# Kernel optimization log

Measured on AMD Instinct MI355X. Metric: run time of the kernel, lower is better.

Reference implementation:

```python
import jax, jax.numpy as jnp
import numpy as np

K_DIM = 256
HEADS = 8


def setup_inputs() -> dict:
    key = jax.random.key(0)
    ks = jax.random.split(key, 6)
    b, t, k, h = 8, 1024, K_DIM, HEADS
    scale = 1.0 / np.sqrt(k)
    x = jax.random.normal(ks[0], (b, t, k), dtype=jnp.float32)
    # nn.Linear(k, k*h, bias=False) weights, stored as (in, out) for x @ W
    Wq = jax.random.normal(ks[1], (k, k * h), dtype=jnp.float32) * scale
    Wk = jax.random.normal(ks[2], (k, k * h), dtype=jnp.float32) * scale
    Wv = jax.random.normal(ks[3], (k, k * h), dtype=jnp.float32) * scale
    # unifyheads: nn.Linear(h*k, k) with bias
    Wu = jax.random.normal(ks[4], (h * k, k), dtype=jnp.float32) * (1.0 / np.sqrt(h * k))
    bu = jax.random.normal(ks[5], (k,), dtype=jnp.float32) * 0.01
    return {"x": x, "Wq": Wq, "Wk": Wk, "Wv": Wv, "Wu": Wu, "bu": bu}


def reference(x, Wq, Wk, Wv, Wu, bu):
    b, t, k = x.shape
    h = Wq.shape[1] // k
    inv4 = 1.0 / (k ** 0.25)  # scale Q and K each by k^(1/4) -> combined 1/sqrt(k)
    q = (x @ Wq).reshape(b, t, h, k) * inv4
    kk = (x @ Wk).reshape(b, t, h, k) * inv4
    v = (x @ Wv).reshape(b, t, h, k)
    # scores: [b, h, t, t]
    scores = jnp.einsum('bthk,bshk->bhts', q, kk)
    att = jax.nn.softmax(scores, axis=-1)
    out = jnp.einsum('bhts,bshk->bthk', att, v).reshape(b, t, h * k)
    return out @ Wu + bu
```

## Files before the change

### kernel.cpp

```cpp
#include <hip/hip_runtime.h>
#include <stdint.h>

typedef unsigned short u16;
typedef __attribute__((ext_vector_type(8))) short bf16x8;
typedef __attribute__((ext_vector_type(4))) float f32x4;

#define LOG2E 1.44269504088896340736f

__device__ __forceinline__ float bf2f(u16 u) {
  union { uint32_t u; float f; } v; v.u = ((uint32_t)u) << 16; return v.f;
}
__device__ __forceinline__ u16 f2bf(float f) {
  union { float f; uint32_t u; } v; v.f = f;
  uint32_t r = v.u + 0x7fffu + ((v.u >> 16) & 1u);
  return (u16)(r >> 16);
}

__device__ __forceinline__ void gl_lds16(const u16* g, u16* l) {
  __builtin_amdgcn_global_load_lds((const __attribute__((address_space(1))) void*)g,
                                   (__attribute__((address_space(3))) void*)l, 16, 0, 0);
}

__device__ __forceinline__ void transpose64f(const float* src, int sstride,
                                             u16* dst, int dstride,
                                             float scale, u16* tile ) {
  const int tid = threadIdx.x;
  const int row = tid >> 3, seg = tid & 7;
#pragma unroll
  for (int p = 0; p < 2; ++p) {
    int rr = p * 32 + row;
    int rw = rr ^ (seg * 8);
    float4 a = *(const float4*)(src + rr * sstride + seg * 8);
    float4 b = *(const float4*)(src + rr * sstride + seg * 8 + 4);
    tile[(seg * 8 + 0) * 80 + rw] = f2bf(a.x * scale);
    tile[(seg * 8 + 1) * 80 + rw] = f2bf(a.y * scale);
    tile[(seg * 8 + 2) * 80 + rw] = f2bf(a.z * scale);
    tile[(seg * 8 + 3) * 80 + rw] = f2bf(a.w * scale);
    tile[(seg * 8 + 4) * 80 + rw] = f2bf(b.x * scale);
    tile[(seg * 8 + 5) * 80 + rw] = f2bf(b.y * scale);
    tile[(seg * 8 + 6) * 80 + rw] = f2bf(b.z * scale);
    tile[(seg * 8 + 7) * 80 + rw] = f2bf(b.w * scale);
  }
  __syncthreads();
#pragma unroll
  for (int p = 0; p < 2; ++p) {
    int rr = p * 32 + row;
    int sw = (seg ^ ((rr >> 3) & 7)) * 8;
    *(uint4*)(dst + rr * dstride + seg * 8) = *(uint4*)(tile + rr * 80 + sw);
  }
}

__global__ __launch_bounds__(256) void k_prep(const float* __restrict__ x,
                                              const float* __restrict__ Wq,
                                              const float* __restrict__ Wk,
                                              const float* __restrict__ Wv,
                                              const float* __restrict__ Wu,
                                              u16* __restrict__ xb,
                                              u16* __restrict__ Wt,
                                              u16* __restrict__ Wut) {
  __shared__ u16 tile[64 * 80];
  const int bx = blockIdx.x;
  if (bx < 2048) {
    const int i = bx * 256 + threadIdx.x;
    float4 v = ((const float4*)x)[i];
    ushort4 o;
    o.x = f2bf(v.x); o.y = f2bf(v.y); o.z = f2bf(v.z); o.w = f2bf(v.w);
    ((ushort4*)xb)[i] = o;
  } else if (bx < 2432) {
    const int idx = bx - 2048;
    const int o0 = (idx % 96) * 64, i0 = (idx / 96) * 64;
    const float* src; float scale = 0.25f; int oc0 = o0;
    if (o0 < 2048)      { src = Wq; }
    else if (o0 < 4096) { src = Wk; oc0 = o0 - 2048; }
    else                { src = Wv; oc0 = o0 - 4096; scale = 1.0f; }
    transpose64f(src + i0 * 2048 + oc0, 2048, Wt + o0 * 256 + i0, 256, scale, tile);
  } else {
    const int idx = bx - 2432;
    const int c0 = (idx % 4) * 64, r0 = (idx / 4) * 64;
    transpose64f(Wu + r0 * 256 + c0, 256, Wut + c0 * 2048 + r0, 2048, 1.0f, tile);
  }
}

__global__ __launch_bounds__(256) void k_gemm_qkv(const u16* __restrict__ A,
                                                  const u16* __restrict__ Bt,
                                                  u16* __restrict__ C,
                                                  u16* __restrict__ vt) {
  __shared__ u16 As[128 * 32];
  __shared__ u16 Bs[128 * 32];
  const int m0 = blockIdx.y * 128, n0 = blockIdx.x * 128;
  const int tid = threadIdx.x, w = tid >> 6, lane = tid & 63;
  const int q = lane >> 4, r = lane & 15;
  const int wm = (w >> 1) * 64, wn = (w & 1) * 64;
  const int bo0 = w * 2048 + lane * 16;
  const int row0 = bo0 >> 6, col0 = (bo0 & 63) >> 1;
  const int bo1 = bo0 + 1024;
  const int row1 = bo1 >> 6, col1 = (bo1 & 63) >> 1;
  f32x4 acc[4][4] = {};
  for (int kt = 0; kt < 256; kt += 32) {
    __syncthreads();
    gl_lds16(A + (m0 + row0) * 256 + kt + col0, As + w * 1024);
    gl_lds16(A + (m0 + row1) * 256 + kt + col1, As + w * 1024 + 512);
    gl_lds16(Bt + (n0 + row0) * 256 + kt + col0, Bs + w * 1024);
    gl_lds16(Bt + (n0 + row1) * 256 + kt + col1, Bs + w * 1024 + 512);
    __syncthreads();
    bf16x8 af[4], bf[4];
#pragma unroll
    for (int mb = 0; mb < 4; ++mb) af[mb] = *(const bf16x8*)(As + (wm + mb * 16 + r) * 32 + q * 8);
#pragma unroll
    for (int nb = 0; nb < 4; ++nb) bf[nb] = *(const bf16x8*)(Bs + (wn + nb * 16 + r) * 32 + q * 8);
#pragma unroll
    for (int mb = 0; mb < 4; ++mb)
#pragma unroll
      for (int nb = 0; nb < 4; ++nb)
        acc[mb][nb] = __builtin_amdgcn_mfma_f32_16x16x32_bf16(af[mb], bf[nb], acc[mb][nb], 0, 0, 0);
  }
  if (n0 < 4096) {
#pragma unroll
    for (int mb = 0; mb < 4; ++mb)
#pragma unroll
      for (int nb = 0; nb < 4; ++nb) {
        const int nn = n0 + wn + nb * 16 + r;
#pragma unroll
        for (int reg = 0; reg < 4; ++reg) {
          const int mm = m0 + wm + mb * 16 + q * 4 + reg;
          C[(size_t)mm * 6144 + nn] = f2bf(acc[mb][nb][reg]);
        }
      }
  } else {
#pragma unroll
    for (int mb = 0; mb < 4; ++mb)
#pragma unroll
      for (int nb = 0; nb < 4; ++nb) {
        const int hd = n0 - 4096 + wn + nb * 16 + r;
        const int mm0 = m0 + wm + mb * 16 + q * 4;
        const int bb = mm0 >> 10, t = mm0 & 1023;
        uint2 val;
        val.x = (uint32_t)f2bf(acc[mb][nb][0]) | ((uint32_t)f2bf(acc[mb][nb][1]) << 16);
        val.y = (uint32_t)f2bf(acc[mb][nb][2]) | ((uint32_t)f2bf(acc[mb][nb][3]) << 16);
        *(uint2*)(vt + ((size_t)(bb * 2048 + hd)) * 1024 + t) = val;
      }
  }
}

__global__ __launch_bounds__(256, 2) void k_attn(const u16* __restrict__ qkv,
                                                 const u16* __restrict__ vt,
                                                 u16* __restrict__ att) {
  __shared__ u16 smem[17152];
  const int blk = blockIdx.x;
  const int qt = blk >> 6, bh = blk & 63;
  const int b = bh >> 3, h = bh & 7;
  const int tid = threadIdx.x, w = tid >> 6, lane = tid & 63;
  const int q = lane >> 4, r = lane & 15;
  const int t0 = qt * 128 + w * 32;

  const u16* QgA = qkv + ((size_t)(b * 1024 + t0 + r)) * 6144 + h * 256;
  const u16* QgB = QgA + (size_t)16 * 6144;
  bf16x8 qfA[8], qfB[8];
#pragma unroll
  for (int kc = 0; kc < 8; ++kc) {
    qfA[kc] = *(const bf16x8*)(QgA + kc * 32 + q * 8);
    qfB[kc] = *(const bf16x8*)(QgB + kc * 32 + q * 8);
  }

  float lA = 0.0f, lB = 0.0f;
  f32x4 oA[16] = {}, oB[16] = {};

  const u16* Kg = qkv + (size_t)b * 1024 * 6144 + 2048 + h * 256;
  const u16* Vg = vt + (size_t)(b * 8 + h) * 256 * 1024;

  const int kc_s = (tid & 31) >> 2, kq_s = tid & 3;
  const int db_s = tid >> 4, vr_s = tid & 15;

  for (int sc = 0; sc < 1024; sc += 32) {
    __syncthreads();
    {
      uint4 kv[4];
#pragma unroll
      for (int p = 0; p < 4; ++p) {
        int key = p * 8 + (tid >> 5);
        kv[p] = *(const uint4*)(Kg + (size_t)(sc + key) * 6144 + (tid & 31) * 8);
      }
#pragma unroll
      for (int p = 0; p < 4; ++p) {
        int key = p * 8 + (tid >> 5);
        int sb = key >> 4, kr = key & 15;
        int unit = (kc_s * 2 + sb) * 64 + kq_s * 16 + ((kr + kq_s + kc_s * 4) & 15);
        *(uint4*)(smem + unit * 8) = kv[p];
      }
    }
    {
      uint4 vv[4];
#pragma unroll
      for (int p = 0; p < 4; ++p)
        vv[p] = *(const uint4*)(Vg + (size_t)tid * 1024 + sc + p * 8);
#pragma unroll
      for (int p = 0; p < 4; ++p) {
        int unit = db_s * 64 + p * 16 + ((vr_s + p) & 15);
        *(uint4*)(smem + 8192 + unit * 8) = vv[p];
      }
    }
    __syncthreads();

    f32x4 s0A = {}, s1A = {}, s0B = {}, s1B = {};
#pragma unroll
    for (int kc = 0; kc < 8; ++kc) {
      bf16x8 k0 = *(const bf16x8*)(smem + ((kc * 2 + 0) * 64 + q * 16 + ((r + q + kc * 4) & 15)) * 8);
      bf16x8 k1 = *(const bf16x8*)(smem + ((kc * 2 + 1) * 64 + q * 16 + ((r + q + kc * 4) & 15)) * 8);
      s0A = __builtin_amdgcn_mfma_f32_16x16x32_bf16(k0, qfA[kc], s0A, 0, 0, 0);
      s1A = __builtin_amdgcn_mfma_f32_16x16x32_bf16(k1, qfA[kc], s1A, 0, 0, 0);
      s0B = __builtin_amdgcn_mfma_f32_16x16x32_bf16(k0, qfB[kc], s0B, 0, 0, 0);
      s1B = __builtin_amdgcn_mfma_f32_16x16x32_bf16(k1, qfB[kc], s1B, 0, 0, 0);
    }

    union { bf16x8 v; u16 e[8]; } pfA, pfB;
    {
      float pa[4], pb[4];
#pragma unroll
      for (int reg = 0; reg < 4; ++reg) {
        pa[reg] = exp2f(s0A[reg] * LOG2E);
        pb[reg] = exp2f(s1A[reg] * LOG2E);
        lA += pa[reg] + pb[reg];
      }
      uint32_t pk[4];
#pragma unroll
      for (int reg = 0; reg < 4; ++reg)
        pk[reg] = (uint32_t)f2bf(pa[reg]) | ((uint32_t)f2bf(pb[reg]) << 16);
      const int srcA = ((q & 1) << 5) + r, srcB = srcA + 16;
      uint32_t tt[8];
#pragma unroll
      for (int reg = 0; reg < 4; ++reg) tt[reg] = (uint32_t)__shfl((int)pk[reg], srcA);
#pragma unroll
      for (int reg = 0; reg < 4; ++reg) tt[4 + reg] = (uint32_t)__shfl((int)pk[reg], srcB);
      const bool hi = (q >= 2);
#pragma unroll
      for (int j = 0; j < 8; ++j)
        pfA.e[j] = hi ? (u16)(tt[j] >> 16) : (u16)(tt[j] & 0xffffu);
    }
    {
      float pa[4], pb[4];
#pragma unroll
      for (int reg = 0; reg < 4; ++reg) {
        pa[reg] = exp2f(s0B[reg] * LOG2E);
        pb[reg] = exp2f(s1B[reg] * LOG2E);
        lB += pa[reg] + pb[reg];
      }
      uint32_t pk[4];
#pragma unroll
      for (int reg = 0; reg < 4; ++reg)
        pk[reg] = (uint32_t)f2bf(pa[reg]) | ((uint32_t)f2bf(pb[reg]) << 16);
      const int srcA = ((q & 1) << 5) + r, srcB = srcA + 16;
      uint32_t tt[8];
#pragma unroll
      for (int reg = 0; reg < 4; ++reg) tt[reg] = (uint32_t)__shfl((int)pk[reg], srcA);
#pragma unroll
      for (int reg = 0; reg < 4; ++reg) tt[4 + reg] = (uint32_t)__shfl((int)pk[reg], srcB);
      const bool hi = (q >= 2);
#pragma unroll
      for (int j = 0; j < 8; ++j)
        pfB.e[j] = hi ? (u16)(tt[j] >> 16) : (u16)(tt[j] & 0xffffu);
    }

#pragma unroll
    for (int db = 0; db < 16; ++db) {
      bf16x8 vf = *(const bf16x8*)(smem + 8192 + (db * 64 + q * 16 + ((r + q) & 15)) * 8);
      oA[db] = __builtin_amdgcn_mfma_f32_16x16x32_bf16(vf, pfA.v, oA[db], 0, 0, 0);
      oB[db] = __builtin_amdgcn_mfma_f32_16x16x32_bf16(vf, pfB.v, oB[db], 0, 0, 0);
    }
  }

  lA += __shfl_xor(lA, 16); lA += __shfl_xor(lA, 32);
  lB += __shfl_xor(lB, 16); lB += __shfl_xor(lB, 32);
  float rlA = 1.0f / lA, rlB = 1.0f / lB;

  __syncthreads();
  u16* Os = smem + w * 4288;
#pragma unroll
  for (int pass = 0; pass < 2; ++pass) {
    const f32x4* o = pass ? oB : oA;
    const float rl = pass ? rlB : rlA;
    const int tb = t0 + pass * 16;
    __syncthreads();
#pragma unroll
    for (int db = 0; db < 16; ++db) {
      uint32_t lo = (uint32_t)f2bf(o[db][0] * rl) | ((uint32_t)f2bf(o[db][1] * rl) << 16);
      uint32_t hi2 = (uint32_t)f2bf(o[db][2] * rl) | ((uint32_t)f2bf(o[db][3] * rl) << 16);
      uint2 val; val.x = lo; val.y = hi2;
      *(uint2*)(Os + r * 268 + db * 16 + q * 4) = val;
    }
    asm volatile("s_waitcnt lgkmcnt(0)" ::: "memory");
    u16* Ag = att + ((size_t)(b * 1024 + tb)) * 2048 + h * 256;
#pragma unroll
    for (int p = 0; p < 8; ++p) {
      int idx = (p * 64 + lane) * 8;
      int row = idx >> 8, col = idx & 255;
      *(uint4*)(Ag + (size_t)row * 2048 + col) = *(uint4*)(Os + row * 268 + col);
    }
  }
}

__global__ __launch_bounds__(256) void k_gemm_out(const u16* __restrict__ A,
                                                  const u16* __restrict__ Bt,
                                                  const float* __restrict__ bu,
                                                  float* __restrict__ C) {
  __shared__ u16 As[64 * 32];
  __shared__ u16 Bs[64 * 32];
  const int m0 = blockIdx.y * 64, n0 = blockIdx.x * 64;
  const int tid = threadIdx.x, w = tid >> 6, lane = tid & 63;
  const int q = lane >> 4, r = lane & 15;
  const int wm = (w >> 1) * 32, wn = (w & 1) * 32;
  const int bo = w * 1024 + lane * 16;
  const int rw = bo >> 6, cl = (bo & 63) >> 1;
  f32x4 acc[2][2] = {};
  for (int kt = 0; kt < 2048; kt += 32) {
    __syncthreads();
    gl_lds16(A + (size_t)(m0 + rw) * 2048 + kt + cl, As + w * 512);
    gl_lds16(Bt + (size_t)(n0 + rw) * 2048 + kt + cl, Bs + w * 512);
    __syncthreads();
    bf16x8 af[2], bf[2];
#pragma unroll
    for (int mb = 0; mb < 2; ++mb) af[mb] = *(const bf16x8*)(As + (wm + mb * 16 + r) * 32 + q * 8);
#pragma unroll
    for (int nb = 0; nb < 2; ++nb) bf[nb] = *(const bf16x8*)(Bs + (wn + nb * 16 + r) * 32 + q * 8);
#pragma unroll
    for (int mb = 0; mb < 2; ++mb)
#pragma unroll
      for (int nb = 0; nb < 2; ++nb)
        acc[mb][nb] = __builtin_amdgcn_mfma_f32_16x16x32_bf16(af[mb], bf[nb], acc[mb][nb], 0, 0, 0);
  }
  float bias[2];
#pragma unroll
  for (int nb = 0; nb < 2; ++nb) bias[nb] = bu[n0 + wn + nb * 16 + r];
#pragma unroll
  for (int mb = 0; mb < 2; ++mb)
#pragma unroll
    for (int nb = 0; nb < 2; ++nb) {
      const int nn = n0 + wn + nb * 16 + r;
#pragma unroll
      for (int reg = 0; reg < 4; ++reg) {
        const int mm = m0 + wm + mb * 16 + q * 4 + reg;
        C[(size_t)mm * 256 + nn] = acc[mb][nb][reg] + bias[nb];
      }
    }
}

extern "C" void kernel_launch(void* const* d_in, const int* in_sizes, int n_in,
                              void* d_out, int out_size, void* d_ws, size_t ws_size,
                              hipStream_t stream) {
  const float* x  = (const float*)d_in[0];
  const float* Wq = (const float*)d_in[1];
  const float* Wk = (const float*)d_in[2];
  const float* Wv = (const float*)d_in[3];
  const float* Wu = (const float*)d_in[4];
  const float* bu = (const float*)d_in[5];
  float* outp = (float*)d_out;

  char* ws = (char*)d_ws;
  u16* qkv   = (u16*)(ws);
  u16* vt    = (u16*)(ws + 100663296);
  u16* attb  = (u16*)(ws + 134217728);
  u16* wqkvt = (u16*)(ws + 167772160);
  u16* wut   = (u16*)(ws + 170917888);
  u16* xb    = (u16*)(ws + 171966464);
  (void)in_sizes; (void)n_in; (void)out_size; (void)ws_size;

  dim3 blk(256);
  k_prep<<<dim3(2560), blk, 0, stream>>>(x, Wq, Wk, Wv, Wu, xb, wqkvt, wut);
  k_gemm_qkv<<<dim3(48, 64), blk, 0, stream>>>(xb, wqkvt, qkv, vt);
  k_attn<<<dim3(512), blk, 0, stream>>>(qkv, vt, attb);
  k_gemm_out<<<dim3(4, 128), blk, 0, stream>>>(attb, wut, bu, outp);
}
```

Baseline: 267.8 us.

## Double-buffer K/V tiles in LDS via async global_load_lds prefetch

Result: slower. 282.7 us (+5.6%).

```diff
diff --git a/kernel.cpp b/kernel.cpp
--- a/kernel.cpp
+++ b/kernel.cpp
@@ -145,7 +145,7 @@
 __global__ __launch_bounds__(256, 2) void k_attn(const u16* __restrict__ qkv,
                                                  const u16* __restrict__ vt,
                                                  u16* __restrict__ att) {
-  __shared__ u16 smem[17152];
+  __shared__ u16 smem[32768];
   const int blk = blockIdx.x;
   const int qt = blk >> 6, bh = blk & 63;
   const int b = bh >> 3, h = bh & 7;
@@ -168,44 +168,49 @@
   const u16* Kg = qkv + (size_t)b * 1024 * 6144 + 2048 + h * 256;
   const u16* Vg = vt + (size_t)(b * 8 + h) * 256 * 1024;
 
-  const int kc_s = (tid & 31) >> 2, kq_s = tid & 3;
-  const int db_s = tid >> 4, vr_s = tid & 15;
-
-  for (int sc = 0; sc < 1024; sc += 32) {
-    __syncthreads();
-    {
-      uint4 kv[4];
-#pragma unroll
-      for (int p = 0; p < 4; ++p) {
-        int key = p * 8 + (tid >> 5);
-        kv[p] = *(const uint4*)(Kg + (size_t)(sc + key) * 6144 + (tid & 31) * 8);
-      }
-#pragma unroll
-      for (int p = 0; p < 4; ++p) {
-        int key = p * 8 + (tid >> 5);
-        int sb = key >> 4, kr = key & 15;
-        int unit = (kc_s * 2 + sb) * 64 + kq_s * 16 + ((kr + kq_s + kc_s * 4) & 15);
-        *(uint4*)(smem + unit * 8) = kv[p];
-      }
-    }
-    {
-      uint4 vv[4];
-#pragma unroll
-      for (int p = 0; p < 4; ++p)
-        vv[p] = *(const uint4*)(Vg + (size_t)tid * 1024 + sc + p * 8);
-#pragma unroll
-      for (int p = 0; p < 4; ++p) {
-        int unit = db_s * 64 + p * 16 + ((vr_s + p) & 15);
-        *(uint4*)(smem + 8192 + unit * 8) = vv[p];
-      }
-    }
-    __syncthreads();
+#pragma unroll
+  for (int j = 0; j < 4; ++j) {
+    const int e = w * 4 + j;
+    const int key = (e << 1) | (lane >> 5);
+    const int dsg = ((lane & 31) - key) & 31;
+    gl_lds16(Kg + (size_t)key * 6144 + dsg * 8, smem + e * 512);
+    const int d = (e << 4) + (lane >> 2);
+    const int ks = ((lane & 3) - (d >> 1)) & 3;
+    gl_lds16(Vg + (size_t)d * 1024 + ks * 8, smem + 16384 + e * 512);
+  }
+
+  const int kb0 = (r >> 1) * 64 + (r & 1) * 32;
+  const int kb1 = kb0 + 512;
+  const int rot0 = q + r;
+  const int rot1 = q + r + 16;
+  const int vb = 4 * r + ((q + (r >> 1)) & 3);
+
+  for (int it = 0; it < 32; ++it) {
+    asm volatile("s_waitcnt vmcnt(0)" ::: "memory");
+    __syncthreads();
+    const int cur = it & 1;
+    if (it + 1 < 32) {
+      const int scn = (it + 1) * 32;
+      const int nxt = cur ^ 1;
+#pragma unroll
+      for (int j = 0; j < 4; ++j) {
+        const int e = w * 4 + j;
+        const int key = (e << 1) | (lane >> 5);
+        const int dsg = ((lane & 31) - key) & 31;
+        gl_lds16(Kg + (size_t)(scn + key) * 6144 + dsg * 8, smem + nxt * 8192 + e * 512);
+        const int d = (e << 4) + (lane >> 2);
+        const int ks = ((lane & 3) - (d >> 1)) & 3;
+        gl_lds16(Vg + (size_t)d * 1024 + scn + ks * 8, smem + 16384 + nxt * 8192 + e * 512);
+      }
+    }
+    const u16* Kc = smem + cur * 8192;
+    const u16* Vc = smem + 16384 + cur * 8192;
 
     f32x4 s0A = {}, s1A = {}, s0B = {}, s1B = {};
 #pragma unroll
     for (int kc = 0; kc < 8; ++kc) {
-      bf16x8 k0 = *(const bf16x8*)(smem + ((kc * 2 + 0) * 64 + q * 16 + ((r + q + kc * 4) & 15)) * 8);
-      bf16x8 k1 = *(const bf16x8*)(smem + ((kc * 2 + 1) * 64 + q * 16 + ((r + q + kc * 4) & 15)) * 8);
+      bf16x8 k0 = *(const bf16x8*)(Kc + (kb0 + ((rot0 + 4 * kc) & 31)) * 8);
+      bf16x8 k1 = *(const bf16x8*)(Kc + (kb1 + ((rot1 + 4 * kc) & 31)) * 8);
       s0A = __builtin_amdgcn_mfma_f32_16x16x32_bf16(k0, qfA[kc], s0A, 0, 0, 0);
       s1A = __builtin_amdgcn_mfma_f32_16x16x32_bf16(k1, qfA[kc], s1A, 0, 0, 0);
       s0B = __builtin_amdgcn_mfma_f32_16x16x32_bf16(k0, qfB[kc], s0B, 0, 0, 0);
@@ -262,7 +267,7 @@
 
 #pragma unroll
     for (int db = 0; db < 16; ++db) {
-      bf16x8 vf = *(const bf16x8*)(smem + 8192 + (db * 64 + q * 16 + ((r + q) & 15)) * 8);
+      bf16x8 vf = *(const bf16x8*)(Vc + (db * 64 + vb) * 8);
       oA[db] = __builtin_amdgcn_mfma_f32_16x16x32_bf16(vf, pfA.v, oA[db], 0, 0, 0);
       oB[db] = __builtin_amdgcn_mfma_f32_16x16x32_bf16(vf, pfB.v, oB[db], 0, 0, 0);
     }
```
